# Performance work log

Hardware: AMD Instinct MI355X
Metric: run time of the kernel (lower is better)

The kernel has to match this reference:

```python
import jax, jax.numpy as jnp
import numpy as np

NUM_USERS = 100000
NUM_ITEMS = 100000
D = 64
B, P, N, NB, NN = 1024, 32, 64, 32, 32
W1, W2, W3 = 1.0, 0.1, 1.0


def setup_inputs() -> dict:
    key = jax.random.key(0)
    ks = jax.random.split(key, 12)
    u2e = 0.1 + 0.03 * jax.random.normal(ks[0], (NUM_USERS, D), jnp.float32)
    v2e = 0.1 + 0.03 * jax.random.normal(ks[1], (NUM_ITEMS, D), jnp.float32)
    margin_uv = jnp.ones((NUM_USERS, 1), jnp.float32)
    margin_vv = jnp.ones((NUM_ITEMS, 1), jnp.float32)
    margin_uu = jnp.ones((NUM_USERS, 1), jnp.float32)
    train_u = jax.random.randint(ks[2], (B,), 0, NUM_USERS)
    pos_idx = jax.random.randint(ks[3], (B, P), 0, NUM_ITEMS)
    neg_idx = jax.random.randint(ks[4], (B, N), 0, NUM_ITEMS)
    nb_idx = jax.random.randint(ks[5], (B, NB), 0, NUM_USERS)
    nn_idx = jax.random.randint(ks[6], (B, NN), 0, NUM_USERS)
    # ragged lengths -> padded masks
    def mk_mask(k, maxlen):
        lens = jax.random.randint(k, (B,), 1, maxlen + 1)
        return jnp.arange(maxlen)[None, :] < lens[:, None]
    pos_mask = mk_mask(ks[7], P)
    neg_mask = mk_mask(ks[8], N)
    nb_mask = mk_mask(ks[9], NB)
    nn_mask = mk_mask(ks[10], NN)
    return dict(u2e=u2e, v2e=v2e, margin_uv=margin_uv, margin_vv=margin_vv,
                margin_uu=margin_uu, train_u=train_u, pos_idx=pos_idx,
                neg_idx=neg_idx, nb_idx=nb_idx, nn_idx=nn_idx,
                pos_mask=pos_mask, neg_mask=neg_mask, nb_mask=nb_mask,
                nn_mask=nn_mask)


def reference(u2e, v2e, margin_uv, margin_vv, margin_uu, train_u, pos_idx,
              neg_idx, nb_idx, nn_idx, pos_mask, neg_mask, nb_mask, nn_mask):
    u_e = u2e[train_u]            # [B,D]
    p_e = v2e[pos_idx]            # [B,P,D]
    n_e = v2e[neg_idx]            # [B,N,D]
    nb_e = u2e[nb_idx]            # [B,NB,D]
    nn_e = u2e[nn_idx]            # [B,NN,D]
    pm = pos_mask.astype(u_e.dtype)
    nm = neg_mask.astype(u_e.dtype)
    nbm = nb_mask.astype(u_e.dtype)
    nnm = nn_mask.astype(u_e.dtype)

    # user-item triplet loss: hinge[b,i,k] = m_u[b] + ||u-p_i||^2 - ||u-n_k||^2
    d1 = jnp.sum((u_e[:, None, :] - p_e) ** 2, -1)   # [B,P]
    d2 = jnp.sum((u_e[:, None, :] - n_e) ** 2, -1)   # [B,N]
    m_u = margin_uv[train_u, 0]                       # [B]
    uv = jax.nn.relu(m_u[:, None, None] + d1[:, :, None] - d2[:, None, :])
    uv_loss = jnp.sum(uv * (pm[:, :, None] * nm[:, None, :]))

    # item-item loss (torch broadcast: margin over a separate positive axis j)
    # hinge[b,i,j,k] = m_v[b,j] + ||p_i-u||^2 - ||p_i-n_k||^2
    p2 = jnp.sum(p_e ** 2, -1)                        # [B,P]
    n2 = jnp.sum(n_e ** 2, -1)                        # [B,N]
    d2v = p2[:, :, None] + n2[:, None, :] - 2.0 * jnp.einsum('bpd,bnd->bpn', p_e, n_e)
    m_v = margin_vv[pos_idx, 0]                       # [B,P]
    hinge_vv = jax.nn.relu(m_v[:, None, :, None] + d1[:, :, None, None] - d2v[:, :, None, :])
    mask_vv = pm[:, :, None, None] * pm[:, None, :, None] * nm[:, None, None, :]
    vv_loss = jnp.sum(hinge_vv * mask_vv)

    # user-user social loss
    d1s = jnp.sum((u_e[:, None, :] - nb_e) ** 2, -1)  # [B,NB]
    d2s = jnp.sum((u_e[:, None, :] - nn_e) ** 2, -1)  # [B,NN]
    m_s = margin_uu[train_u, 0]                       # [B]
    uu = jax.nn.relu(m_s[:, None, None] + d1s[:, :, None] - d2s[:, None, :])
    uu_loss = jnp.sum(uu * (nbm[:, :, None] * nnm[:, None, :]))

    # margin regularizer (masked mean over batch positives)
    loss_am = (jnp.mean(margin_uv[train_u])
               + jnp.sum(m_v * pm) / jnp.sum(pm)
               + jnp.mean(margin_uu[train_u]))

    return uv_loss + W1 * vv_loss + W3 * uu_loss + W2 * loss_am
```

## Files before the change

kernel.cpp:

```cpp
#include <hip/hip_runtime.h>
#include <cfloat>

#define BB   1024
#define PP   32
#define NNEG 64
#define DD   64
#define BSTR 72
#define SSTR 66

static constexpr float W2c = 0.1f;

typedef __attribute__((ext_vector_type(8)))  short bf16x8;
typedef __attribute__((ext_vector_type(16))) float f32x16;

__device__ __forceinline__ short f2bf(float f) {
    unsigned u = __float_as_uint(f);
    unsigned r = (u + 0x7fffu + ((u >> 16) & 1u)) >> 16;
    return (short)r;
}

__device__ __forceinline__ float parse_mask(const void* p, int flag, int j) {
    if (flag == 1) return ((const unsigned char*)p)[j] ? 1.0f : 0.0f;
    if (flag == 2) return (((const float*)p)[j] != 0.0f) ? 1.0f : 0.0f;
    return ((const int*)p)[j] ? 1.0f : 0.0f;
}

__global__ __launch_bounds__(512, 8) void loss_kernel(
    const float* __restrict__ u2e, const float* __restrict__ v2e,
    const float* __restrict__ margin_uv, const float* __restrict__ margin_vv,
    const float* __restrict__ margin_uu,
    const int* __restrict__ train_u, const int* __restrict__ pos_idx,
    const int* __restrict__ neg_idx, const int* __restrict__ nb_idx,
    const int* __restrict__ nn_idx,
    const void* __restrict__ pos_mask, const void* __restrict__ neg_mask,
    const void* __restrict__ nb_mask, const void* __restrict__ nn_mask,
    float* __restrict__ ws) {

    const int b = blockIdx.x;
    const int t = threadIdx.x;
    const int lane = t & 63;
    const int w = t >> 6;

    __shared__ __align__(16) short pn_bf[96 * BSTR];
    __shared__ __align__(16) float s_lds[PP * SSTR];
    __shared__ __align__(16) float u_s[DD];
    __shared__ float d1[PP], p2s[PP], d2[NNEG], n2s[NNEG], d1sA[PP], d2sA[PP];
    __shared__ float pmf[PP], nmf[NNEG], nbmf[PP], nnmf[PP];
    __shared__ float mvp[PP], mv_arr[PP], s_srt[PP], S_suf[PP + 1];
    __shared__ int   pos_i[PP], neg_i[NNEG], nb_i[PP], nn_i[PP];
    __shared__ float sc[2];
    __shared__ float red[8][3];
    __shared__ int   wflags[8][2];

    const int tu = train_u[b];

    {
        unsigned int mw = ((const unsigned int*)pos_mask)[t];
        int f32hit  = (mw == 0x3f800000u) ? 1 : 0;
        int bytehit = (!f32hit && (mw & 0xFFFFFF00u)) ? 1 : 0;
        int wf = __any(f32hit) ? 1 : 0;
        int wb = __any(bytehit) ? 1 : 0;
        if (lane == 0) { wflags[w][0] = wf; wflags[w][1] = wb; }
    }
    if (t < DD) u_s[t] = u2e[(size_t)tu * DD + t];
    if (t < PP)              pos_i[t]       = pos_idx[b * PP + t];
    else if (t < 96)         neg_i[t - PP]  = neg_idx[b * NNEG + (t - PP)];
    else if (t < 128)        nb_i[t - 96]   = nb_idx[b * PP + (t - 96)];
    else if (t < 160)        nn_i[t - 128]  = nn_idx[b * PP + (t - 128)];
    if (t == 0) { sc[0] = margin_uv[tu]; sc[1] = margin_uu[tu]; }
    __syncthreads();

    const int flag = (wflags[0][0] | wflags[1][0] | wflags[2][0] | wflags[3][0] |
                      wflags[4][0] | wflags[5][0] | wflags[6][0] | wflags[7][0]) ? 2
                   : ((wflags[0][1] | wflags[1][1] | wflags[2][1] | wflags[3][1] |
                       wflags[4][1] | wflags[5][1] | wflags[6][1] | wflags[7][1]) ? 1 : 0);

    const int q  = t & 15;
    const int R0 = t >> 4;
    const float4 u4 = *(const float4*)(u_s + 4 * q);
    float4 ch[3];
    float sdp[3], sqp[3];
    #pragma unroll
    for (int r = 0; r < 3; ++r) {
        const int R = R0 + 32 * r;
        const int gidx = (R < PP) ? pos_i[R] : neg_i[R - PP];
        ch[r] = *(const float4*)(v2e + (size_t)gidx * DD + 4 * q);
        float dx = ch[r].x - u4.x, dy = ch[r].y - u4.y,
              dz = ch[r].z - u4.z, dw = ch[r].w - u4.w;
        sdp[r] = dx * dx + dy * dy + dz * dz + dw * dw;
        sqp[r] = ch[r].x * ch[r].x + ch[r].y * ch[r].y
               + ch[r].z * ch[r].z + ch[r].w * ch[r].w;
    }
    #pragma unroll
    for (int m = 1; m < 16; m <<= 1) {
        #pragma unroll
        for (int r = 0; r < 3; ++r) {
            sdp[r] += __shfl_xor(sdp[r], m);
            sqp[r] += __shfl_xor(sqp[r], m);
        }
    }
    if (q == 0) {
        #pragma unroll
        for (int r = 0; r < 3; ++r) {
            const int R = R0 + 32 * r;
            if (R < PP) { d1[R] = sdp[r]; p2s[R] = sqp[r]; }
            else        { d2[R - PP] = sdp[r]; n2s[R - PP] = sqp[r]; }
        }
    }
    if (t < PP) {
        float pm = parse_mask(pos_mask, flag, b * PP + t);
        float mv = margin_vv[pos_i[t]];
        pmf[t] = pm; mv_arr[t] = mv;
        mvp[t] = (pm != 0.0f) ? mv : -FLT_MAX;
    } else if (t < 96) {
        nmf[t - PP] = parse_mask(neg_mask, flag, b * NNEG + (t - PP));
    } else if (t < 128) {
        nbmf[t - 96] = parse_mask(nb_mask, flag, b * PP + (t - 96));
    } else if (t < 160) {
        nnmf[t - 128] = parse_mask(nn_mask, flag, b * PP + (t - 128));
    }
    {
        const int row = t >> 3, sub = t & 7;
        const int idx = (row < PP) ? nb_i[row] : nn_i[row - PP];
        const float* rp = u2e + (size_t)idx * DD + 8 * sub;
        float4 e0 = *(const float4*)(rp);
        float4 e1 = *(const float4*)(rp + 4);
        float4 v0 = *(const float4*)(u_s + 8 * sub);
        float4 v1 = *(const float4*)(u_s + 8 * sub + 4);
        float dx = e0.x - v0.x, dy = e0.y - v0.y, dz = e0.z - v0.z, dw = e0.w - v0.w;
        float s = dx * dx + dy * dy + dz * dz + dw * dw;
        dx = e1.x - v1.x; dy = e1.y - v1.y; dz = e1.z - v1.z; dw = e1.w - v1.w;
        s += dx * dx + dy * dy + dz * dz + dw * dw;
        s += __shfl_xor(s, 1);
        s += __shfl_xor(s, 2);
        s += __shfl_xor(s, 4);
        if (sub == 0) { if (row < PP) d1sA[row] = s; else d2sA[row - PP] = s; }
    }
    #pragma unroll
    for (int r = 0; r < 3; ++r) {
        const int R = R0 + 32 * r;
        short4 s4 = make_short4(f2bf(ch[r].x), f2bf(ch[r].y), f2bf(ch[r].z), f2bf(ch[r].w));
        *(short4*)(pn_bf + R * BSTR + 4 * q) = s4;
    }
    __syncthreads();

    if (w < 2) {
        f32x16 acc;
        #pragma unroll
        for (int i = 0; i < 16; ++i) acc[i] = 0.0f;
        const int lr = lane & 31;
        const int hi = lane >> 5;
        const short* ap = pn_bf + lr * BSTR;
        const short* bp = pn_bf + (PP + 32 * w + lr) * BSTR;
        #pragma unroll
        for (int c = 0; c < 4; ++c) {
            const int d0 = 16 * c + 8 * hi;
            bf16x8 a   = *(const bf16x8*)(ap + d0);
            bf16x8 bfr = *(const bf16x8*)(bp + d0);
            acc = __builtin_amdgcn_mfma_f32_32x32x16_bf16(a, bfr, acc, 0, 0, 0);
        }
        #pragma unroll
        for (int r = 0; r < 16; ++r) {
            const int m = (r & 3) + 8 * (r >> 2) + 4 * hi;
            s_lds[m * SSTR + 32 * w + lr] = acc[r];
        }
    } else if (w == 2 && lane < PP) {
        float vj = mvp[lane];
        int r = 0;
        #pragma unroll
        for (int j = 0; j < PP; ++j) {
            float o = mvp[j];
            r += (o < vj || (o == vj && j < lane)) ? 1 : 0;
        }
        s_srt[r] = vj;
        __threadfence_block();
        float y = s_srt[lane];
        #pragma unroll
        for (int d = 1; d < PP; d <<= 1) {
            float z = __shfl_down(y, d);
            if (lane + d < PP) y += z;
        }
        S_suf[lane] = y;
        if (lane == 0) S_suf[PP] = 0.0f;
    }
    __syncthreads();

    const float m_u = sc[0], m_s = sc[1];
    const float s31 = s_srt[PP - 1];
    const int kb = t & 15;
    const int i  = t >> 4;
    const float d1i = d1[i], p2i = p2s[i], pmi = pmf[i];
    float loss = 0.0f;
    #pragma unroll
    for (int c = 0; c < 4; ++c) {
        const int k = kb + 16 * c;
        const float Sik = s_lds[i * SSTR + k];
        const float cc = d1i - (p2i + n2s[k] - 2.0f * Sik);
        const float v = -cc;
        int t0 = 0;
        #pragma unroll
        for (int st = 16; st > 0; st >>= 1)
            t0 += (s_srt[t0 + st - 1] <= v) ? st : 0;
        t0 += (s31 <= v) ? 1 : 0;
        const float inner = S_suf[t0] + (float)(PP - t0) * cc;
        const float uvh = fmaxf(m_u + d1i - d2[k], 0.0f);
        loss += pmi * nmf[k] * (inner + uvh);
    }

    #pragma unroll
    for (int rr = 0; rr < 2; ++rr) {
        int pid = t + 512 * rr;
        int ii = pid >> 5, k = pid & 31;
        loss += nbmf[ii] * nnmf[k] * fmaxf(m_s + d1sA[ii] - d2sA[k], 0.0f);
    }

    float a2 = (t < PP) ? mv_arr[t] * pmf[t] : 0.0f;
    float a3 = (t < PP) ? pmf[t] : 0.0f;
    #pragma unroll
    for (int m = 1; m < 64; m <<= 1) {
        loss += __shfl_xor(loss, m);
        a2   += __shfl_xor(a2, m);
        a3   += __shfl_xor(a3, m);
    }
    if (lane == 0) { red[w][0] = loss; red[w][1] = a2; red[w][2] = a3; }
    __syncthreads();
    if (t == 0) {
        float S0 = 0, S2 = 0, S3 = 0;
        #pragma unroll
        for (int i2 = 0; i2 < 8; ++i2) { S0 += red[i2][0]; S2 += red[i2][1]; S3 += red[i2][2]; }
        ws[0 * BB + b] = S0;
        ws[1 * BB + b] = sc[0];
        ws[2 * BB + b] = S2;
        ws[3 * BB + b] = S3;
        ws[4 * BB + b] = sc[1];
    }
}

__global__ __launch_bounds__(256) void finalize_kernel(const float* __restrict__ ws,
                                                       float* __restrict__ out) {
    __shared__ float red[4][5];
    const int t = threadIdx.x, lane = t & 63, w = t >> 6;
    float s[5] = {0, 0, 0, 0, 0};
    for (int i = t; i < BB; i += 256)
        #pragma unroll
        for (int a = 0; a < 5; ++a) s[a] += ws[a * BB + i];
    #pragma unroll
    for (int m = 1; m < 64; m <<= 1)
        #pragma unroll
        for (int a = 0; a < 5; ++a) s[a] += __shfl_xor(s[a], m);
    if (lane == 0)
        #pragma unroll
        for (int a = 0; a < 5; ++a) red[w][a] = s[a];
    __syncthreads();
    if (t == 0) {
        float S[5];
        #pragma unroll
        for (int a = 0; a < 5; ++a) {
            S[a] = 0;
            for (int i = 0; i < 4; ++i) S[a] += red[i][a];
        }
        float loss_am = S[1] / (float)BB + S[2] / S[3] + S[4] / (float)BB;
        out[0] = S[0] + W2c * loss_am;
    }
}

extern "C" void kernel_launch(void* const* d_in, const int* in_sizes, int n_in,
                              void* d_out, int out_size, void* d_ws, size_t ws_size,
                              hipStream_t stream) {
    const float* u2e       = (const float*)d_in[0];
    const float* v2e       = (const float*)d_in[1];
    const float* margin_uv = (const float*)d_in[2];
    const float* margin_vv = (const float*)d_in[3];
    const float* margin_uu = (const float*)d_in[4];
    const int*   train_u   = (const int*)d_in[5];
    const int*   pos_idx   = (const int*)d_in[6];
    const int*   neg_idx   = (const int*)d_in[7];
    const int*   nb_idx    = (const int*)d_in[8];
    const int*   nn_idx    = (const int*)d_in[9];
    const void*  pos_mask  = d_in[10];
    const void*  neg_mask  = d_in[11];
    const void*  nb_mask   = d_in[12];
    const void*  nn_mask   = d_in[13];

    float* ws  = (float*)d_ws;
    float* out = (float*)d_out;

    loss_kernel<<<BB, 512, 0, stream>>>(u2e, v2e, margin_uv, margin_vv, margin_uu,
                                        train_u, pos_idx, neg_idx, nb_idx, nn_idx,
                                        pos_mask, neg_mask, nb_mask, nn_mask, ws);
    finalize_kernel<<<1, 256, 0, stream>>>(ws, out);
}
```

Before: 21.37 us.

## Remove initial LDS staging barrier and issue all gathers directly from registers

```diff
diff --git a/kernel.cpp b/kernel.cpp
--- a/kernel.cpp
+++ b/kernel.cpp
@@ -43,73 +43,81 @@
 
     __shared__ __align__(16) short pn_bf[96 * BSTR];
     __shared__ __align__(16) float s_lds[PP * SSTR];
-    __shared__ __align__(16) float u_s[DD];
     __shared__ float d1[PP], p2s[PP], d2[NNEG], n2s[NNEG], d1sA[PP], d2sA[PP];
     __shared__ float pmf[PP], nmf[NNEG], nbmf[PP], nnmf[PP];
     __shared__ float mvp[PP], mv_arr[PP], s_srt[PP], S_suf[PP + 1];
-    __shared__ int   pos_i[PP], neg_i[NNEG], nb_i[PP], nn_i[PP];
     __shared__ float sc[2];
     __shared__ float red[8][3];
-    __shared__ int   wflags[8][2];
-
-    const int tu = train_u[b];
+
+    unsigned f32h = 0, byth = 0;
+    #pragma unroll
+    for (int i2 = 0; i2 < 16; ++i2) {
+        unsigned mw = ((const unsigned int*)pos_mask)[lane + 64 * i2];
+        f32h |= (mw == 0x3f800000u) ? 1u : 0u;
+        byth |= ((mw != 0x3f800000u) && (mw & 0xFFFFFF00u)) ? 1u : 0u;
+    }
+    const int flag = __any(f32h) ? 2 : (__any(byth) ? 1 : 0);
+
+    const int tu  = train_u[b];
+    const int q   = t & 15;
+    const int R0  = t >> 4;
+    const int gi0 = pos_idx[b * PP + R0];
+    const int gi1 = neg_idx[b * NNEG + R0];
+    const int gi2 = neg_idx[b * NNEG + R0 + 32];
+    const int row = t >> 3, sub = t & 7;
+    const int sidx = (row < PP) ? nb_idx[b * PP + row] : nn_idx[b * PP + row - PP];
+
+    const float* uR = u2e + (size_t)tu * DD;
+    const float4 u4 = *(const float4*)(uR + 4 * q);
+    float4 ch0 = *(const float4*)(v2e + (size_t)gi0 * DD + 4 * q);
+    float4 ch1 = *(const float4*)(v2e + (size_t)gi1 * DD + 4 * q);
+    float4 ch2 = *(const float4*)(v2e + (size_t)gi2 * DD + 4 * q);
+    const float* rp = u2e + (size_t)sidx * DD + 8 * sub;
+    const float4 e0 = *(const float4*)(rp);
+    const float4 e1 = *(const float4*)(rp + 4);
+    const float4 v0 = *(const float4*)(uR + 8 * sub);
+    const float4 v1 = *(const float4*)(uR + 8 * sub + 4);
 
     {
-        unsigned int mw = ((const unsigned int*)pos_mask)[t];
-        int f32hit  = (mw == 0x3f800000u) ? 1 : 0;
-        int bytehit = (!f32hit && (mw & 0xFFFFFF00u)) ? 1 : 0;
-        int wf = __any(f32hit) ? 1 : 0;
-        int wb = __any(bytehit) ? 1 : 0;
-        if (lane == 0) { wflags[w][0] = wf; wflags[w][1] = wb; }
-    }
-    if (t < DD) u_s[t] = u2e[(size_t)tu * DD + t];
-    if (t < PP)              pos_i[t]       = pos_idx[b * PP + t];
-    else if (t < 96)         neg_i[t - PP]  = neg_idx[b * NNEG + (t - PP)];
-    else if (t < 128)        nb_i[t - 96]   = nb_idx[b * PP + (t - 96)];
-    else if (t < 160)        nn_i[t - 128]  = nn_idx[b * PP + (t - 128)];
-    if (t == 0) { sc[0] = margin_uv[tu]; sc[1] = margin_uu[tu]; }
-    __syncthreads();
-
-    const int flag = (wflags[0][0] | wflags[1][0] | wflags[2][0] | wflags[3][0] |
-                      wflags[4][0] | wflags[5][0] | wflags[6][0] | wflags[7][0]) ? 2
-                   : ((wflags[0][1] | wflags[1][1] | wflags[2][1] | wflags[3][1] |
-                       wflags[4][1] | wflags[5][1] | wflags[6][1] | wflags[7][1]) ? 1 : 0);
-
-    const int q  = t & 15;
-    const int R0 = t >> 4;
-    const float4 u4 = *(const float4*)(u_s + 4 * q);
-    float4 ch[3];
-    float sdp[3], sqp[3];
-    #pragma unroll
-    for (int r = 0; r < 3; ++r) {
-        const int R = R0 + 32 * r;
-        const int gidx = (R < PP) ? pos_i[R] : neg_i[R - PP];
-        ch[r] = *(const float4*)(v2e + (size_t)gidx * DD + 4 * q);
-        float dx = ch[r].x - u4.x, dy = ch[r].y - u4.y,
-              dz = ch[r].z - u4.z, dw = ch[r].w - u4.w;
-        sdp[r] = dx * dx + dy * dy + dz * dz + dw * dw;
-        sqp[r] = ch[r].x * ch[r].x + ch[r].y * ch[r].y
-               + ch[r].z * ch[r].z + ch[r].w * ch[r].w;
-    }
-    #pragma unroll
-    for (int m = 1; m < 16; m <<= 1) {
-        #pragma unroll
-        for (int r = 0; r < 3; ++r) {
-            sdp[r] += __shfl_xor(sdp[r], m);
-            sqp[r] += __shfl_xor(sqp[r], m);
-        }
-    }
-    if (q == 0) {
-        #pragma unroll
-        for (int r = 0; r < 3; ++r) {
-            const int R = R0 + 32 * r;
-            if (R < PP) { d1[R] = sdp[r]; p2s[R] = sqp[r]; }
-            else        { d2[R - PP] = sdp[r]; n2s[R - PP] = sqp[r]; }
-        }
+        float sdp[3], sqp[3];
+        float4 cc0 = ch0, cc1 = ch1, cc2 = ch2;
+        float dx, dy, dz, dw;
+        dx = cc0.x-u4.x; dy = cc0.y-u4.y; dz = cc0.z-u4.z; dw = cc0.w-u4.w;
+        sdp[0] = dx*dx+dy*dy+dz*dz+dw*dw;
+        sqp[0] = cc0.x*cc0.x+cc0.y*cc0.y+cc0.z*cc0.z+cc0.w*cc0.w;
+        dx = cc1.x-u4.x; dy = cc1.y-u4.y; dz = cc1.z-u4.z; dw = cc1.w-u4.w;
+        sdp[1] = dx*dx+dy*dy+dz*dz+dw*dw;
+        sqp[1] = cc1.x*cc1.x+cc1.y*cc1.y+cc1.z*cc1.z+cc1.w*cc1.w;
+        dx = cc2.x-u4.x; dy = cc2.y-u4.y; dz = cc2.z-u4.z; dw = cc2.w-u4.w;
+        sdp[2] = dx*dx+dy*dy+dz*dz+dw*dw;
+        sqp[2] = cc2.x*cc2.x+cc2.y*cc2.y+cc2.z*cc2.z+cc2.w*cc2.w;
+        #pragma unroll
+        for (int m = 1; m < 16; m <<= 1) {
+            #pragma unroll
+            for (int r = 0; r < 3; ++r) {
+                sdp[r] += __shfl_xor(sdp[r], m);
+                sqp[r] += __shfl_xor(sqp[r], m);
+            }
+        }
+        if (q == 0) {
+            d1[R0]       = sdp[0]; p2s[R0]       = sqp[0];
+            d2[R0]       = sdp[1]; n2s[R0]       = sqp[1];
+            d2[R0 + 32]  = sdp[2]; n2s[R0 + 32]  = sqp[2];
+        }
+    }
+    {
+        float dx = e0.x-v0.x, dy = e0.y-v0.y, dz = e0.z-v0.z, dw = e0.w-v0.w;
+        float s = dx*dx+dy*dy+dz*dz+dw*dw;
+        dx = e1.x-v1.x; dy = e1.y-v1.y; dz = e1.z-v1.z; dw = e1.w-v1.w;
+        s += dx*dx+dy*dy+dz*dz+dw*dw;
+        s += __shfl_xor(s, 1);
+        s += __shfl_xor(s, 2);
+        s += __shfl_xor(s, 4);
+        if (sub == 0) { if (row < PP) d1sA[row] = s; else d2sA[row - PP] = s; }
     }
     if (t < PP) {
         float pm = parse_mask(pos_mask, flag, b * PP + t);
-        float mv = margin_vv[pos_i[t]];
+        float mv = margin_vv[pos_idx[b * PP + t]];
         pmf[t] = pm; mv_arr[t] = mv;
         mvp[t] = (pm != 0.0f) ? mv : -FLT_MAX;
     } else if (t < 96) {
@@ -119,28 +127,14 @@
     } else if (t < 160) {
         nnmf[t - 128] = parse_mask(nn_mask, flag, b * PP + (t - 128));
     }
+    if (t == 0) { sc[0] = margin_uv[tu]; sc[1] = margin_uu[tu]; }
     {
-        const int row = t >> 3, sub = t & 7;
-        const int idx = (row < PP) ? nb_i[row] : nn_i[row - PP];
-        const float* rp = u2e + (size_t)idx * DD + 8 * sub;
-        float4 e0 = *(const float4*)(rp);
-        float4 e1 = *(const float4*)(rp + 4);
-        float4 v0 = *(const float4*)(u_s + 8 * sub);
-        float4 v1 = *(const float4*)(u_s + 8 * sub + 4);
-        float dx = e0.x - v0.x, dy = e0.y - v0.y, dz = e0.z - v0.z, dw = e0.w - v0.w;
-        float s = dx * dx + dy * dy + dz * dz + dw * dw;
-        dx = e1.x - v1.x; dy = e1.y - v1.y; dz = e1.z - v1.z; dw = e1.w - v1.w;
-        s += dx * dx + dy * dy + dz * dz + dw * dw;
-        s += __shfl_xor(s, 1);
-        s += __shfl_xor(s, 2);
-        s += __shfl_xor(s, 4);
-        if (sub == 0) { if (row < PP) d1sA[row] = s; else d2sA[row - PP] = s; }
-    }
-    #pragma unroll
-    for (int r = 0; r < 3; ++r) {
-        const int R = R0 + 32 * r;
-        short4 s4 = make_short4(f2bf(ch[r].x), f2bf(ch[r].y), f2bf(ch[r].z), f2bf(ch[r].w));
-        *(short4*)(pn_bf + R * BSTR + 4 * q) = s4;
+        short4 s0 = make_short4(f2bf(ch0.x), f2bf(ch0.y), f2bf(ch0.z), f2bf(ch0.w));
+        short4 s1 = make_short4(f2bf(ch1.x), f2bf(ch1.y), f2bf(ch1.z), f2bf(ch1.w));
+        short4 s2 = make_short4(f2bf(ch2.x), f2bf(ch2.y), f2bf(ch2.z), f2bf(ch2.w));
+        *(short4*)(pn_bf + R0 * BSTR + 4 * q)        = s0;
+        *(short4*)(pn_bf + (R0 + 32) * BSTR + 4 * q) = s1;
+        *(short4*)(pn_bf + (R0 + 64) * BSTR + 4 * q) = s2;
     }
     __syncthreads();
 
@@ -188,7 +182,7 @@
     const float m_u = sc[0], m_s = sc[1];
     const float s31 = s_srt[PP - 1];
     const int kb = t & 15;
-    const int i  = t >> 4;
+    const int i  = R0;
     const float d1i = d1[i], p2i = p2s[i], pmi = pmf[i];
     float loss = 0.0f;
     #pragma unroll
```

After: 21.48 us. No clear change (+0.5%).
